# Kernel optimization log

Measured on AMD Instinct MI355X. Metric: run time of the kernel, lower is better.

## Reference

```python
import jax, jax.numpy as jnp
import numpy as np

N_NODES = 100000
N_EDGES = 3200000


def setup_inputs() -> dict:
    key = jax.random.key(0)
    ks = jax.random.split(key, 10)
    inp = {
        "x": jax.random.normal(ks[0], (N_NODES, 16), dtype=jnp.float32),
        "edge_index": jax.random.randint(ks[1], (2, N_EDGES), 0, N_NODES, dtype=jnp.int64),
        "W1": jax.random.normal(ks[2], (16, 32), dtype=jnp.float32) * 0.25,
        "b1": jax.random.normal(ks[3], (32,), dtype=jnp.float32) * 0.02,
        "W2": jax.random.normal(ks[4], (32, 32), dtype=jnp.float32) * 0.18,
        "b2": jax.random.normal(ks[5], (32,), dtype=jnp.float32) * 0.02,
        "Wl1": jax.random.normal(ks[6], (32, 32), dtype=jnp.float32) * 0.18,
        "bl1": jax.random.normal(ks[7], (32,), dtype=jnp.float32) * 0.02,
        "Wl4": jax.random.normal(ks[8], (32, 1), dtype=jnp.float32) * 0.18,
        "bl4": jax.random.normal(ks[9], (1,), dtype=jnp.float32) * 0.02,
    }
    return inp


def _gcn_norm(edge_index, n_nodes):
    # PyG GCNConv default: add self-loops, symmetric normalization D^-1/2 A_hat D^-1/2.
    loops = jnp.arange(n_nodes, dtype=edge_index.dtype)
    row = jnp.concatenate([edge_index[0], loops])  # source j
    col = jnp.concatenate([edge_index[1], loops])  # target i
    deg = jax.ops.segment_sum(jnp.ones_like(col, dtype=jnp.float32), col, num_segments=n_nodes)
    dinv = jnp.where(deg > 0, jax.lax.rsqrt(deg), 0.0)
    norm = dinv[row] * dinv[col]  # [E + N]
    return row, col, norm


def _gcn_conv(x, W, b, row, col, norm, n_nodes):
    h = x @ W                                   # [N, out] small GEMM
    msgs = h[row] * norm[:, None]               # irregular gather, [E+N, out]
    out = jax.ops.segment_sum(msgs, col, num_segments=n_nodes)  # scatter-add
    return out + b


def reference(x, edge_index, W1, b1, W2, b2, Wl1, bl1, Wl4, bl4):
    n = x.shape[0]
    row, col, norm = _gcn_norm(edge_index, n)
    h = jax.nn.relu(_gcn_conv(x, W1, b1, row, col, norm, n))
    h = jax.nn.relu(_gcn_conv(h, W2, b2, row, col, norm, n))
    h = jax.nn.relu(h @ Wl1 + bl1)
    return h @ Wl4 + bl4  # [N, 1]
```

## Files before the change

### kernel.cpp

```cpp
#include <hip/hip_runtime.h>
#include <hip/hip_fp16.h>
#include <math.h>


#define BN 512
#define BSH 9
#define NBUF 256
#define EPB 4096
#define EPT 8

__global__ void init_cursor(int* __restrict__ gCursor, int NB, int C) {
    int b = blockIdx.x * blockDim.x + threadIdx.x;
    if (b < NB) gCursor[b] = b * C;
}

__global__ void __launch_bounds__(512)
bucket_scatter(const int* __restrict__ row, const int* __restrict__ col,
               int* __restrict__ gCursor, int* __restrict__ packed,
               int E, int NB, int C) {
    __shared__ int hist[NBUF];
    __shared__ int base[NBUF];
    int t = threadIdx.x;
    int blockBase = blockIdx.x * EPB;
    for (int i = t; i < NB; i += 512) hist[i] = 0;
    __syncthreads();
    int pay[EPT];
    int meta[EPT];
#pragma unroll
    for (int k = 0; k < EPT; ++k) {
        int e = blockBase + k * 512 + t;
        if (e < E) {
            int c = col[e];
            int b = c >> BSH;
            int r = atomicAdd(&hist[b], 1);
            pay[k] = (row[e] << BSH) | (c & (BN - 1));
            meta[k] = (b << 16) | r;
        } else {
            meta[k] = -1;
        }
    }
    __syncthreads();
    for (int b = t; b < NB; b += 512) {
        int c = hist[b];
        base[b] = c ? atomicAdd(&gCursor[b], c) : 0;
    }
    __syncthreads();
#pragma unroll
    for (int k = 0; k < EPT; ++k) {
        int m = meta[k];
        if (m >= 0) {
            int b = m >> 16;
            int pos = base[b] + (m & 0xFFFF);
            if (pos < (b + 1) * C)
                packed[pos] = pay[k];
        }
    }
}

__global__ void __launch_bounds__(1024)
bucket_finalize(const int* __restrict__ packed, const int* __restrict__ gCursor,
                int2* __restrict__ rowRange, int* __restrict__ rowMid,
                float* __restrict__ dinv, int* __restrict__ srcs,
                const float4* __restrict__ x4, __half* __restrict__ xs,
                int N, int C, int halfN) {
    __shared__ int cnt[BN * 2];
    __shared__ int cur[BN * 2];
    __shared__ float sdv[BN];
    __shared__ int wsum[16];
    int bkt = blockIdx.x;
    int t = threadIdx.x;
    int nodeBase = bkt << BSH;
    cnt[t] = 0;
    __syncthreads();
    int beg = bkt * C;
    int end = min(gCursor[bkt], beg + C);
    for (int e = beg + t; e < end; e += 1024) {
        int w = packed[e];
        int key = ((w & (BN - 1)) << 1) | ((w >> BSH) >= halfN ? 1 : 0);
        atomicAdd(&cnt[key], 1);
    }
    __syncthreads();
    int c0 = (t < BN) ? cnt[2 * t] : 0;
    int c1 = (t < BN) ? cnt[2 * t + 1] : 0;
    int s = c0 + c1;
    int lane = t & 63, wv = t >> 6;
    int v = s;
#pragma unroll
    for (int off = 1; off < 64; off <<= 1) {
        int u = __shfl_up(v, off);
        if (lane >= off) v += u;
    }
    if (lane == 63) wsum[wv] = v;
    __syncthreads();
    int addv = 0;
#pragma unroll
    for (int w = 0; w < 16; ++w) addv += (w < wv) ? wsum[w] : 0;
    v += addv;
    if (t < BN) {
        int p = beg + v - s;
        cur[2 * t] = p;
        cur[2 * t + 1] = p + c0;
        float d = rsqrtf((float)s + 1.0f);
        sdv[t] = d;
        int n = nodeBase + t;
        if (n < N) {
            rowRange[n] = make_int2(p, p + s);
            rowMid[n] = p + c0;
            dinv[n] = d;
        }
    }
    __syncthreads();
    for (int e = beg + t; e < end; e += 1024) {
        int w = packed[e];
        int src = w >> BSH;
        int key = ((w & (BN - 1)) << 1) | (src >= halfN ? 1 : 0);
        int pos = atomicAdd(&cur[key], 1);
        srcs[pos] = src;
    }
    {
        int n = t >> 1, hf = t & 1;
        int g = nodeBase + n;
        if (g < N) {
            float d = sdv[n];
            float4 va = x4[(size_t)g * 4 + hf * 2];
            float4 vb = x4[(size_t)g * 4 + hf * 2 + 1];
            __half2 h0 = __floats2half2_rn(va.x * d, va.y * d);
            __half2 h1 = __floats2half2_rn(va.z * d, va.w * d);
            __half2 h2 = __floats2half2_rn(vb.x * d, vb.y * d);
            __half2 h3 = __floats2half2_rn(vb.z * d, vb.w * d);
            uint4 u;
            u.x = *(unsigned*)&h0; u.y = *(unsigned*)&h1;
            u.z = *(unsigned*)&h2; u.w = *(unsigned*)&h3;
            *(uint4*)(xs + (size_t)g * 16 + hf * 8) = u;
        }
    }
}

__device__ __forceinline__ void acc8(float* a, uint4 u) {
    float2 f;
    f = __half22float2(*(const __half2*)&u.x); a[0] += f.x; a[1] += f.y;
    f = __half22float2(*(const __half2*)&u.y); a[2] += f.x; a[3] += f.y;
    f = __half22float2(*(const __half2*)&u.z); a[4] += f.x; a[5] += f.y;
    f = __half22float2(*(const __half2*)&u.w); a[6] += f.x; a[7] += f.y;
}

__device__ __forceinline__ void gather_pipe(float* a, const int* __restrict__ srcs,
                                            const __half* __restrict__ tbl,
                                            int rowHalves, int off8,
                                            int first, int limit, int stride) {
    if (first >= limit) return;
    int cntE = (limit - first + stride - 1) / stride;
    int last = limit - 1;
    int sA = srcs[first];
    int sB = (cntE > 1) ? srcs[first + stride] : 0;
    int i = 0;
    for (; i + 2 <= cntE; i += 2) {
        int nA = srcs[min(first + stride * (i + 2), last)];
        int nB = srcs[min(first + stride * (i + 3), last)];
        uint4 fA = *(const uint4*)(tbl + (size_t)sA * rowHalves + off8 * 8);
        uint4 fB = *(const uint4*)(tbl + (size_t)sB * rowHalves + off8 * 8);
        acc8(a, fA);
        acc8(a, fB);
        sA = nA; sB = nB;
    }
    if (i < cntE)
        acc8(a, *(const uint4*)(tbl + (size_t)sA * rowHalves + off8 * 8));
}

__global__ void __launch_bounds__(256)
gather_conv1(const int2* __restrict__ rowRange, const int* __restrict__ srcs,
             const __half* __restrict__ xs, const float* __restrict__ dinv,
             const float* __restrict__ W1, const float* __restrict__ b1,
             __half* __restrict__ hs1, int N) {
    __shared__ float A[32][17];
    __shared__ float sW[512];
    __shared__ float sb[32];
    int t = threadIdx.x;
    for (int i = t; i < 512; i += 256) sW[i] = W1[i];
    if (t < 32) sb[t] = b1[t];
    int tt = blockIdx.x * 256 + t;
    int node = tt >> 3, q = tt & 7, ln = t >> 3;
    int eo = q >> 1, hf = q & 1;
    float a[8] = {0.f, 0.f, 0.f, 0.f, 0.f, 0.f, 0.f, 0.f};
    float di = 0.f;
    if (node < N) {
        int2 rr = rowRange[node];
        gather_pipe(a, srcs, xs, 16, hf, rr.x + eo, rr.y, 4);
        if (eo == 0)
            acc8(a, *(const uint4*)(xs + (size_t)node * 16 + hf * 8));
        di = dinv[node];
    }
#pragma unroll
    for (int j = 0; j < 8; ++j) {
        a[j] += __shfl_xor(a[j], 2);
        a[j] += __shfl_xor(a[j], 4);
        a[j] *= di;
    }
    if (eo == 0) {
#pragma unroll
        for (int j = 0; j < 8; ++j) A[ln][hf * 8 + j] = a[j];
    }
    __syncthreads();
    if (node < N) {
        int k0 = q * 4;
        float acc[4];
#pragma unroll
        for (int j = 0; j < 4; ++j) acc[j] = sb[k0 + j];
#pragma unroll
        for (int c = 0; c < 16; ++c) {
            float ac = A[ln][c];
#pragma unroll
            for (int j = 0; j < 4; ++j) acc[j] += ac * sW[c * 32 + k0 + j];
        }
        __half2 h0 = __floats2half2_rn(di * fmaxf(acc[0], 0.f),
                                       di * fmaxf(acc[1], 0.f));
        __half2 h1 = __floats2half2_rn(di * fmaxf(acc[2], 0.f),
                                       di * fmaxf(acc[3], 0.f));
        uint2 u;
        u.x = *(unsigned*)&h0; u.y = *(unsigned*)&h1;
        *(uint2*)(hs1 + (size_t)node * 32 + k0) = u;
    }
}

__global__ void __launch_bounds__(256)
gather_conv2_lo(const int2* __restrict__ rowRange, const int* __restrict__ rowMid,
                const int* __restrict__ srcs, const __half* __restrict__ hs1,
                float* __restrict__ A2, int N) {
    int tt = blockIdx.x * 256 + threadIdx.x;
    int node = tt >> 3, q = tt & 7;
    int eo = q >> 2, part = q & 3;
    float a[8] = {0.f, 0.f, 0.f, 0.f, 0.f, 0.f, 0.f, 0.f};
    if (node < N) {
        int beg = rowRange[node].x, mid = rowMid[node];
        gather_pipe(a, srcs, hs1, 32, part, beg + eo, mid, 2);
    }
#pragma unroll
    for (int j = 0; j < 8; ++j) a[j] += __shfl_xor(a[j], 4);
    if (node < N && eo == 0) {
        float4 r0, r1;
        r0.x = a[0]; r0.y = a[1]; r0.z = a[2]; r0.w = a[3];
        r1.x = a[4]; r1.y = a[5]; r1.z = a[6]; r1.w = a[7];
        *(float4*)(A2 + (size_t)node * 32 + part * 8) = r0;
        *(float4*)(A2 + (size_t)node * 32 + part * 8 + 4) = r1;
    }
}

__global__ void __launch_bounds__(256)
gather_conv2_hi_head(const int2* __restrict__ rowRange, const int* __restrict__ rowMid,
                     const int* __restrict__ srcs, const __half* __restrict__ hs1,
                     const float* __restrict__ A2, const float* __restrict__ dinv,
                     const float* __restrict__ W2, const float* __restrict__ b2,
                     const float* __restrict__ Wl1, const float* __restrict__ bl1,
                     const float* __restrict__ Wl4, const float* __restrict__ bl4,
                     float* __restrict__ out, int N) {
    __shared__ float A[32][33];
    __shared__ float sW2[1024];
    __shared__ float sWl1[1024];
    __shared__ float sb2[32], sbl1[32], sWl4[32];
    __shared__ float sbl4;
    int t = threadIdx.x;
    for (int i = t; i < 1024; i += 256) { sW2[i] = W2[i]; sWl1[i] = Wl1[i]; }
    if (t < 32) { sb2[t] = b2[t]; sbl1[t] = bl1[t]; sWl4[t] = Wl4[t]; }
    if (t == 0) sbl4 = bl4[0];
    int tt = blockIdx.x * 256 + t;
    int node = tt >> 3, q = tt & 7, ln = t >> 3;
    int eo = q >> 2, part = q & 3;
    float a[8] = {0.f, 0.f, 0.f, 0.f, 0.f, 0.f, 0.f, 0.f};
    if (node < N) {
        int mid = rowMid[node], end = rowRange[node].y;
        gather_pipe(a, srcs, hs1, 32, part, mid + eo, end, 2);
        if (eo == 0)
            acc8(a, *(const uint4*)(hs1 + (size_t)node * 32 + part * 8));
    }
#pragma unroll
    for (int j = 0; j < 8; ++j) a[j] += __shfl_xor(a[j], 4);
    if (node < N && eo == 0) {
        float4 l0 = *(const float4*)(A2 + (size_t)node * 32 + part * 8);
        float4 l1 = *(const float4*)(A2 + (size_t)node * 32 + part * 8 + 4);
        a[0] += l0.x; a[1] += l0.y; a[2] += l0.z; a[3] += l0.w;
        a[4] += l1.x; a[5] += l1.y; a[6] += l1.z; a[7] += l1.w;
        float di = dinv[node];
#pragma unroll
        for (int j = 0; j < 8; ++j) a[j] *= di;
#pragma unroll
        for (int j = 0; j < 8; ++j) A[ln][part * 8 + j] = a[j];
    }
    __syncthreads();
    int k0 = q * 4;
    float h2[4];
#pragma unroll
    for (int j = 0; j < 4; ++j) h2[j] = sb2[k0 + j];
#pragma unroll
    for (int c = 0; c < 32; ++c) {
        float ac = A[ln][c];
#pragma unroll
        for (int j = 0; j < 4; ++j) h2[j] += ac * sW2[c * 32 + k0 + j];
    }
#pragma unroll
    for (int j = 0; j < 4; ++j) h2[j] = fmaxf(h2[j], 0.f);
    __syncthreads();
#pragma unroll
    for (int j = 0; j < 4; ++j) A[ln][k0 + j] = h2[j];
    __syncthreads();
    float h3[4];
#pragma unroll
    for (int j = 0; j < 4; ++j) h3[j] = sbl1[k0 + j];
#pragma unroll
    for (int c = 0; c < 32; ++c) {
        float ac = A[ln][c];
#pragma unroll
        for (int j = 0; j < 4; ++j) h3[j] += ac * sWl1[c * 32 + k0 + j];
    }
    float p = 0.f;
#pragma unroll
    for (int j = 0; j < 4; ++j) p += fmaxf(h3[j], 0.f) * sWl4[k0 + j];
    p += __shfl_xor(p, 1);
    p += __shfl_xor(p, 2);
    p += __shfl_xor(p, 4);
    if (q == 0 && node < N) out[node] = p + sbl4;
}

extern "C" void kernel_launch(void* const* d_in, const int* in_sizes, int n_in,
                              void* d_out, int out_size, void* d_ws, size_t ws_size,
                              hipStream_t stream) {
    const float* x   = (const float*)d_in[0];
    const int*   ei  = (const int*)d_in[1];
    const float* W1  = (const float*)d_in[2];
    const float* b1  = (const float*)d_in[3];
    const float* W2  = (const float*)d_in[4];
    const float* b2  = (const float*)d_in[5];
    const float* Wl1 = (const float*)d_in[6];
    const float* bl1 = (const float*)d_in[7];
    const float* Wl4 = (const float*)d_in[8];
    const float* bl4 = (const float*)d_in[9];
    float* out = (float*)d_out;

    const int N = in_sizes[0] / 16;
    const int E = in_sizes[1] / 2;
    const int* row = ei;
    const int* col = ei + E;
    const int NB = (N + BN - 1) >> BSH;
    const int halfN = N / 2;
    int C = (E + NB - 1) / NB;
    C = (C * 9 + 7) / 8;
    C = (C + 63) & ~63;

    char* ws = (char*)d_ws;
    auto align = [](size_t v) { return (v + 511) & ~(size_t)511; };
    size_t o = 0;
    int*    gCursor  = (int*)(ws + o);    o = align(o + (size_t)NBUF * 4);
    int2*   rowRange = (int2*)(ws + o);   o = align(o + (size_t)N * 8);
    int*    rowMid   = (int*)(ws + o);    o = align(o + (size_t)N * 4);
    float*  dinv     = (float*)(ws + o);  o = align(o + (size_t)N * 4);
    int*    packed   = (int*)(ws + o);    o = align(o + (size_t)NB * C * 4);
    int*    srcs     = (int*)(ws + o);    o = align(o + (size_t)NB * C * 4);
    __half* xs       = (__half*)(ws + o); o = align(o + (size_t)N * 16 * 2);
    __half* hs1      = (__half*)(ws + o); o = align(o + (size_t)N * 32 * 2);
    float*  A2       = (float*)(ws + o);  o = align(o + (size_t)N * 32 * 4);

    const int BLK = 256;
    int gridSc = (E + EPB - 1) / EPB;
    int gridG8 = (N * 8 + BLK - 1) / BLK;

    init_cursor<<<1, BLK, 0, stream>>>(gCursor, NB, C);
    bucket_scatter<<<gridSc, 512, 0, stream>>>(row, col, gCursor, packed, E, NB, C);
    bucket_finalize<<<NB, 1024, 0, stream>>>(packed, gCursor, rowRange, rowMid, dinv,
                                             srcs, (const float4*)x, xs, N, C, halfN);

    gather_conv1<<<gridG8, BLK, 0, stream>>>(rowRange, srcs, xs, dinv, W1, b1, hs1, N);

    gather_conv2_lo<<<gridG8, BLK, 0, stream>>>(rowRange, rowMid, srcs, hs1, A2, N);
    gather_conv2_hi_head<<<gridG8, BLK, 0, stream>>>(rowRange, rowMid, srcs, hs1, A2,
                                                     dinv, W2, b2, Wl1, bl1,
                                                     Wl4, bl4, out, N);
}
```

Before: 214.7 us.

## Halve bucket size, stage bucket sort and edge indices in LDS

Buckets now hold 256 nodes instead of 512 (512 buckets). In finalize, the per-bucket counting sort writes into shared memory first and then copies out to global contiguously, replacing scattered global writes. The three gather kernels preload each block's contiguous source-index range into LDS when it fits, and fall back to global indices when it does not. This adds LDS pressure, which may reduce occupancy, and adds an extra sync and copy phase.

```diff
diff --git a/kernel.cpp b/kernel.cpp
--- a/kernel.cpp
+++ b/kernel.cpp
@@ -3,11 +3,13 @@
 #include <math.h>
 
 
-#define BN 512
-#define BSH 9
-#define NBUF 256
+#define BN 256
+#define BSH 8
+#define NBUF 512
 #define EPB 4096
 #define EPT 8
+#define CMAX 10240
+#define SLDS 1536
 
 __global__ void init_cursor(int* __restrict__ gCursor, int NB, int C) {
     int b = blockIdx.x * blockDim.x + threadIdx.x;
@@ -67,13 +69,15 @@
     __shared__ int cur[BN * 2];
     __shared__ float sdv[BN];
     __shared__ int wsum[16];
+    __shared__ int sorted[CMAX];
     int bkt = blockIdx.x;
     int t = threadIdx.x;
     int nodeBase = bkt << BSH;
-    cnt[t] = 0;
+    if (t < BN * 2) cnt[t] = 0;
     __syncthreads();
     int beg = bkt * C;
     int end = min(gCursor[bkt], beg + C);
+    int m = end - beg;
     for (int e = beg + t; e < end; e += 1024) {
         int w = packed[e];
         int key = ((w & (BN - 1)) << 1) | ((w >> BSH) >= halfN ? 1 : 0);
@@ -97,30 +101,35 @@
     for (int w = 0; w < 16; ++w) addv += (w < wv) ? wsum[w] : 0;
     v += addv;
     if (t < BN) {
-        int p = beg + v - s;
+        int p = v - s;
         cur[2 * t] = p;
         cur[2 * t + 1] = p + c0;
         float d = rsqrtf((float)s + 1.0f);
         sdv[t] = d;
         int n = nodeBase + t;
         if (n < N) {
-            rowRange[n] = make_int2(p, p + s);
-            rowMid[n] = p + c0;
+            rowRange[n] = make_int2(beg + p, beg + p + s);
+            rowMid[n] = beg + p + c0;
             dinv[n] = d;
         }
     }
     __syncthreads();
+    bool useLds = (m <= CMAX);
     for (int e = beg + t; e < end; e += 1024) {
         int w = packed[e];
         int src = w >> BSH;
         int key = ((w & (BN - 1)) << 1) | (src >= halfN ? 1 : 0);
         int pos = atomicAdd(&cur[key], 1);
-        srcs[pos] = src;
-    }
+        if (useLds) sorted[pos] = src;
+        else        srcs[beg + pos] = src;
+    }
+    __syncthreads();
+    if (useLds)
+        for (int i = t; i < m; i += 1024) srcs[beg + i] = sorted[i];
     {
         int n = t >> 1, hf = t & 1;
         int g = nodeBase + n;
-        if (g < N) {
+        if (t < BN * 2 && g < N) {
             float d = sdv[n];
             float4 va = x4[(size_t)g * 4 + hf * 2];
             float4 vb = x4[(size_t)g * 4 + hf * 2 + 1];
@@ -144,19 +153,19 @@
     f = __half22float2(*(const __half2*)&u.w); a[6] += f.x; a[7] += f.y;
 }
 
-__device__ __forceinline__ void gather_pipe(float* a, const int* __restrict__ srcs,
+__device__ __forceinline__ void gather_pipe(float* a, const int* __restrict__ idx,
                                             const __half* __restrict__ tbl,
                                             int rowHalves, int off8,
                                             int first, int limit, int stride) {
     if (first >= limit) return;
     int cntE = (limit - first + stride - 1) / stride;
     int last = limit - 1;
-    int sA = srcs[first];
-    int sB = (cntE > 1) ? srcs[first + stride] : 0;
+    int sA = idx[first];
+    int sB = (cntE > 1) ? idx[first + stride] : 0;
     int i = 0;
     for (; i + 2 <= cntE; i += 2) {
-        int nA = srcs[min(first + stride * (i + 2), last)];
-        int nB = srcs[min(first + stride * (i + 3), last)];
+        int nA = idx[min(first + stride * (i + 2), last)];
+        int nB = idx[min(first + stride * (i + 3), last)];
         uint4 fA = *(const uint4*)(tbl + (size_t)sA * rowHalves + off8 * 8);
         uint4 fB = *(const uint4*)(tbl + (size_t)sB * rowHalves + off8 * 8);
         acc8(a, fA);
@@ -175,9 +184,18 @@
     __shared__ float A[32][17];
     __shared__ float sW[512];
     __shared__ float sb[32];
+    __shared__ int sIdx[SLDS];
     int t = threadIdx.x;
     for (int i = t; i < 512; i += 256) sW[i] = W1[i];
     if (t < 32) sb[t] = b1[t];
+    int node0 = blockIdx.x * 32;
+    int lastN = min(node0 + 31, N - 1);
+    int base = rowRange[node0].x;
+    int tot = rowRange[lastN].y - base;
+    bool useLds = (tot <= SLDS);
+    if (useLds)
+        for (int i = t; i < tot; i += 256) sIdx[i] = srcs[base + i];
+    __syncthreads();
     int tt = blockIdx.x * 256 + t;
     int node = tt >> 3, q = tt & 7, ln = t >> 3;
     int eo = q >> 1, hf = q & 1;
@@ -185,7 +203,10 @@
     float di = 0.f;
     if (node < N) {
         int2 rr = rowRange[node];
-        gather_pipe(a, srcs, xs, 16, hf, rr.x + eo, rr.y, 4);
+        if (useLds)
+            gather_pipe(a, sIdx, xs, 16, hf, rr.x - base + eo, rr.y - base, 4);
+        else
+            gather_pipe(a, srcs, xs, 16, hf, rr.x + eo, rr.y, 4);
         if (eo == 0)
             acc8(a, *(const uint4*)(xs + (size_t)node * 16 + hf * 8));
         di = dinv[node];
@@ -226,13 +247,26 @@
 gather_conv2_lo(const int2* __restrict__ rowRange, const int* __restrict__ rowMid,
                 const int* __restrict__ srcs, const __half* __restrict__ hs1,
                 float* __restrict__ A2, int N) {
-    int tt = blockIdx.x * 256 + threadIdx.x;
+    __shared__ int sIdx[SLDS];
+    int t = threadIdx.x;
+    int node0 = blockIdx.x * 32;
+    int lastN = min(node0 + 31, N - 1);
+    int base = rowRange[node0].x;
+    int tot = rowRange[lastN].y - base;
+    bool useLds = (tot <= SLDS);
+    if (useLds)
+        for (int i = t; i < tot; i += 256) sIdx[i] = srcs[base + i];
+    __syncthreads();
+    int tt = blockIdx.x * 256 + t;
     int node = tt >> 3, q = tt & 7;
     int eo = q >> 2, part = q & 3;
     float a[8] = {0.f, 0.f, 0.f, 0.f, 0.f, 0.f, 0.f, 0.f};
     if (node < N) {
         int beg = rowRange[node].x, mid = rowMid[node];
-        gather_pipe(a, srcs, hs1, 32, part, beg + eo, mid, 2);
+        if (useLds)
+            gather_pipe(a, sIdx, hs1, 32, part, beg - base + eo, mid - base, 2);
+        else
+            gather_pipe(a, srcs, hs1, 32, part, beg + eo, mid, 2);
     }
 #pragma unroll
     for (int j = 0; j < 8; ++j) a[j] += __shfl_xor(a[j], 4);
@@ -258,17 +292,29 @@
     __shared__ float sWl1[1024];
     __shared__ float sb2[32], sbl1[32], sWl4[32];
     __shared__ float sbl4;
+    __shared__ int sIdx[SLDS];
     int t = threadIdx.x;
     for (int i = t; i < 1024; i += 256) { sW2[i] = W2[i]; sWl1[i] = Wl1[i]; }
     if (t < 32) { sb2[t] = b2[t]; sbl1[t] = bl1[t]; sWl4[t] = Wl4[t]; }
     if (t == 0) sbl4 = bl4[0];
+    int node0 = blockIdx.x * 32;
+    int lastN = min(node0 + 31, N - 1);
+    int base = rowRange[node0].x;
+    int tot = rowRange[lastN].y - base;
+    bool useLds = (tot <= SLDS);
+    if (useLds)
+        for (int i = t; i < tot; i += 256) sIdx[i] = srcs[base + i];
+    __syncthreads();
     int tt = blockIdx.x * 256 + t;
     int node = tt >> 3, q = tt & 7, ln = t >> 3;
     int eo = q >> 2, part = q & 3;
     float a[8] = {0.f, 0.f, 0.f, 0.f, 0.f, 0.f, 0.f, 0.f};
     if (node < N) {
         int mid = rowMid[node], end = rowRange[node].y;
-        gather_pipe(a, srcs, hs1, 32, part, mid + eo, end, 2);
+        if (useLds)
+            gather_pipe(a, sIdx, hs1, 32, part, mid - base + eo, end - base, 2);
+        else
+            gather_pipe(a, srcs, hs1, 32, part, mid + eo, end, 2);
         if (eo == 0)
             acc8(a, *(const uint4*)(hs1 + (size_t)node * 32 + part * 8));
     }
@@ -361,8 +407,9 @@
     const int BLK = 256;
     int gridSc = (E + EPB - 1) / EPB;
     int gridG8 = (N * 8 + BLK - 1) / BLK;
-
-    init_cursor<<<1, BLK, 0, stream>>>(gCursor, NB, C);
+    int gridIc = (NB + BLK - 1) / BLK;
+
+    init_cursor<<<gridIc, BLK, 0, stream>>>(gCursor, NB, C);
     bucket_scatter<<<gridSc, 512, 0, stream>>>(row, col, gCursor, packed, E, NB, C);
     bucket_finalize<<<NB, 1024, 0, stream>>>(packed, gCursor, rowRange, rowMid, dinv,
                                              srcs, (const float4*)x, xs, N, C, halfN);
```

Result: faster. 198.1 us (-7.7%).
